# Kernel optimization log

Measured on AMD Instinct MI355X. Metric: run time of the kernel, lower is better.

The kernel has to match this reference:

```python
import jax, jax.numpy as jnp
import numpy as np
import math

SEQ = 45000
FEAT = 30
DEPTH, HEADS, DK, MLP, C = 4, 4, 32, 512, 32
MAXSEQ = 512


def pos_embed_table():
    # Enformer-style basis functions over distances [-SEQ+1, SEQ-1]
    d = jnp.arange(-SEQ + 1, SEQ, dtype=jnp.float32)
    a = jnp.abs(d)[:, None]
    nb = FEAT // 6  # basis per class (exponential / central-mask / gamma)
    # exponential decay
    hl = 2.0 ** jnp.linspace(3.0, math.log(SEQ) / math.log(2.0), nb)
    e1 = jnp.exp(-math.log(2.0) / hl[None, :] * a)
    # central mask
    cw = 2.0 ** jnp.arange(1, nb + 1, dtype=jnp.float32) - 1.0
    e2 = (cw[None, :] > a).astype(jnp.float32)
    # gamma pdf
    stddev = SEQ / (2 * nb)
    start_mean = SEQ / nb
    mean = jnp.linspace(start_mean, float(SEQ), nb)
    conc = (mean / stddev) ** 2
    rate = mean / stddev ** 2
    logp = jax.scipy.special.xlogy(conc - 1.0, a) - rate * a
    logz = jax.scipy.special.gammaln(conc) - conc * jnp.log(rate)
    p = jnp.exp(logp - logz) + 1e-8
    e3 = p / jnp.max(p)
    e = jnp.concatenate([e1, e2, e3], axis=-1)
    return jnp.concatenate([e, jnp.sign(d)[:, None] * e], axis=-1)  # [2*SEQ-1, FEAT]


def layernorm(x, g, b, eps=1e-5):
    mu = jnp.mean(x, axis=-1, keepdims=True)
    var = jnp.var(x, axis=-1, keepdims=True)
    return (x - mu) * jax.lax.rsqrt(var + eps) * g + b


def setup_inputs() -> dict:
    key = jax.random.key(0)
    ks = jax.random.split(key, 16)
    B, L = 2, SEQ
    HD = HEADS * DK
    s = 0.02
    return {
        "x_skip": jax.random.normal(ks[0], (B, C, L), jnp.float32),
        "attention": jax.random.uniform(ks[1], (B, 3, L), jnp.float32),
        "ln1_g": jnp.ones((DEPTH, C), jnp.float32),
        "ln1_b": jnp.zeros((DEPTH, C), jnp.float32),
        "Wq": jax.random.normal(ks[2], (DEPTH, C, HD), jnp.float32) * s,
        "Wk": jax.random.normal(ks[3], (DEPTH, C, HD), jnp.float32) * s,
        "Wv": jax.random.normal(ks[4], (DEPTH, C, HD), jnp.float32) * s,
        "Wrel": jax.random.normal(ks[5], (DEPTH, FEAT, HD), jnp.float32) * s,
        "rcb": jax.random.normal(ks[6], (DEPTH, HEADS, DK), jnp.float32),
        "rpb": jax.random.normal(ks[7], (DEPTH, HEADS, DK), jnp.float32),
        "Wo": jax.random.normal(ks[8], (DEPTH, HD, C), jnp.float32) * s,
        "bo": jnp.zeros((DEPTH, C), jnp.float32),
        "ln2_g": jnp.ones((DEPTH, C), jnp.float32),
        "ln2_b": jnp.zeros((DEPTH, C), jnp.float32),
        "W1": jax.random.normal(ks[9], (DEPTH, C, MLP), jnp.float32) * s,
        "b1": jnp.zeros((DEPTH, MLP), jnp.float32),
        "W2": jax.random.normal(ks[10], (DEPTH, MLP, C), jnp.float32) * s,
        "b2": jnp.zeros((DEPTH, C), jnp.float32),
    }


def reference(x_skip, attention, ln1_g, ln1_b, Wq, Wk, Wv, Wrel, rcb, rpb, Wo, bo, ln2_g, ln2_b, W1, b1, W2, b2):
    B, Cc, L = x_skip.shape
    half = MAXSEQ // 2
    x_emb = jnp.swapaxes(x_skip, 1, 2)  # [B, L, C]
    # top splice sites by acceptor / donor score
    acc = jnp.argsort(-attention[:, 1, :], axis=1)[:, :half]
    don = jnp.argsort(-attention[:, 2, :], axis=1)[:, :half]
    idx = jnp.sort(jnp.concatenate([acc, don], axis=1), axis=1)  # [B, n]
    n = idx.shape[1]
    diff = idx[:, :, None] - idx[:, None, :] + SEQ - 1  # [B, n, n]
    positions = pos_embed_table()[diff]  # [B, n, n, FEAT]
    emb = jnp.take_along_axis(x_emb, idx[:, :, None], axis=1)  # [B, n, C]
    scale = DK ** -0.5
    for l in range(DEPTH):
        h = layernorm(emb, ln1_g[l], ln1_b[l])
        q = (h @ Wq[l]).reshape(B, n, HEADS, DK).transpose(0, 2, 1, 3) * scale
        k = (h @ Wk[l]).reshape(B, n, HEADS, DK).transpose(0, 2, 1, 3)
        v = (h @ Wv[l]).reshape(B, n, HEADS, DK).transpose(0, 2, 1, 3)
        content = jnp.einsum('bhid,bhjd->bhij', q + rcb[l][None, :, None, :], k)
        rel_k = (positions @ Wrel[l]).reshape(B, n, n, HEADS, DK)  # b i j h d
        rel = jnp.einsum('bhid,bijhd->bhij', q + rpb[l][None, :, None, :], rel_k)
        attn_w = jax.nn.softmax(content + rel, axis=-1)
        o = jnp.einsum('bhij,bhjd->bhid', attn_w, v)
        o = o.transpose(0, 2, 1, 3).reshape(B, n, HEADS * DK)
        emb = emb + o @ Wo[l] + bo[l]
        h2 = layernorm(emb, ln2_g[l], ln2_b[l])
        emb = emb + jax.nn.gelu(h2 @ W1[l] + b1[l], approximate=False) @ W2[l] + b2[l]
    out = jnp.zeros_like(x_emb).at[jnp.arange(B)[:, None], idx].set(emb)
    return jnp.swapaxes(out, 1, 2)  # [B, C, L]
```

## Files before the change

### kernel.cpp

```cpp
#include <hip/hip_runtime.h>
#include <math.h>

#define SEQL   45000
#define NBAT   2
#define CCH    32
#define NSEL   512
#define NHEAD  4
#define DKD    32
#define HDD    128
#define MLPD   512
#define CDCAP  2048
#define TKB    32
#define ETB    176

__device__ __forceinline__ unsigned short f2bf(float x) {
  unsigned u = __float_as_uint(x);
  u = (u + 0x7fffu + ((u >> 16) & 1u)) >> 16;
  return (unsigned short)u;
}
#define BFL(u) __uint_as_float((u) << 16)
#define BFH(u) __uint_as_float((u) & 0xffff0000u)
#define U8F(w, s) ((float)(((w) >> (s)) & 0xffu))

__global__ __launch_bounds__(256) void prep_kernel(const float* __restrict__ att,
                                                   unsigned char* __restrict__ E,
                                                   int* __restrict__ hist,
                                                   float* __restrict__ out) {
  {
    int nthr = gridDim.x * 256;
    int gt = blockIdx.x * 256 + threadIdx.x;
    float4 z4 = make_float4(0.f, 0.f, 0.f, 0.f);
    float4* o4 = (float4*)out;
    for (int i = gt; i < NBAT * CCH * SEQL / 4; i += nthr) o4[i] = z4;
  }
  if (blockIdx.x < ETB) {
    int a = blockIdx.x * 256 + threadIdx.x;
    if (a >= SEQL) return;
    float ad = (float)a;
    float outv[16];
    float log2S = log2f((float)SEQL);
    #pragma unroll
    for (int k = 0; k < 5; ++k) {
      float hl = exp2f(3.0f + (float)k * (log2S - 3.0f) * 0.25f);
      outv[k] = exp2f(-ad / hl);
    }
    const int cw[5] = {1, 3, 7, 15, 31};
    #pragma unroll
    for (int k = 0; k < 5; ++k) outv[5 + k] = (a < cw[k]) ? 1.0f : 0.0f;
    float pmax = 0.0f;
    float pk[5];
    #pragma unroll
    for (int k = 0; k < 5; ++k) {
      float mean = 9000.0f * (float)(k + 1);
      float sd = 4500.0f;
      float cc = (mean / sd) * (mean / sd);
      float rr = mean / (sd * sd);
      float logz = lgammaf(cc) - cc * logf(rr);
      float pp;
      if (a == 0) pp = 1e-8f;
      else pp = expf((cc - 1.0f) * logf(ad) - rr * ad - logz) + 1e-8f;
      pk[k] = pp;
      float mstar = (cc - 1.0f) / rr;
      float m0 = floorf(mstar), m1 = m0 + 1.0f;
      if (m1 > (float)(SEQL - 1)) m1 = (float)(SEQL - 1);
      float p0 = expf((cc - 1.0f) * logf(m0) - rr * m0 - logz) + 1e-8f;
      float p1 = expf((cc - 1.0f) * logf(m1) - rr * m1 - logz) + 1e-8f;
      pmax = fmaxf(pmax, fmaxf(p0, p1));
    }
    #pragma unroll
    for (int k = 0; k < 5; ++k) outv[10 + k] = pk[k] / pmax;
    outv[15] = 0.0f;
    unsigned by[16];
    #pragma unroll
    for (int k = 0; k < 15; ++k)
      by[k] = (unsigned)(fminf(fmaxf(outv[k], 0.f), 1.f) * 255.f + 0.5f);
    by[15] = 0u;
    uint4 o;
    o.x = by[0]  | (by[1]  << 8) | (by[2]  << 16) | (by[3]  << 24);
    o.y = by[4]  | (by[5]  << 8) | (by[6]  << 16) | (by[7]  << 24);
    o.z = by[8]  | (by[9]  << 8) | (by[10] << 16) | (by[11] << 24);
    o.w = by[12] | (by[13] << 8) | (by[14] << 16);
    *(uint4*)(E + (size_t)a * 16) = o;
  } else {
    int bid = blockIdx.x - ETB;
    int ch4 = bid / TKB;
    int blk = bid % TKB;
    int b = ch4 >> 1, ch = ch4 & 1;
    const float* row = att + ((size_t)b * 3 + 1 + ch) * SEQL;
    int* h = hist + (size_t)ch4 * 65536;
    int per = (SEQL + TKB - 1) / TKB;
    int lo = blk * per;
    int hi = lo + per; if (hi > SEQL) hi = SEQL;
    for (int i = lo + threadIdx.x; i < hi; i += 256)
      atomicAdd(&h[__float_as_uint(row[i]) >> 16], 1);
  }
}

__global__ __launch_bounds__(256) void topk_collect_kernel(
    const float* __restrict__ att, const int* __restrict__ hist,
    unsigned long long* __restrict__ cand, int* __restrict__ cnt) {
  __shared__ int s_scan[256];
  __shared__ int s_aux[2];
  int tid = threadIdx.x;
  int ch4 = blockIdx.x / TKB;
  int blk = blockIdx.x % TKB;
  const int* h = hist + (size_t)ch4 * 65536;
  {
    int base = tid * 256;
    int sum = 0;
    for (int i = 0; i < 64; ++i) {
      int4 v = ((const int4*)(h + base))[i];
      sum += v.x + v.y + v.z + v.w;
    }
    s_scan[tid] = sum;
  }
  __syncthreads();
  for (int d = 1; d < 256; d <<= 1) {
    int v = s_scan[tid] + ((tid + d < 256) ? s_scan[tid + d] : 0);
    __syncthreads();
    s_scan[tid] = v;
    __syncthreads();
  }
  {
    int sufEx = (tid == 255) ? 0 : s_scan[tid + 1];
    if (s_scan[tid] >= 256 && sufEx < 256) { s_aux[0] = tid; s_aux[1] = 256 - sufEx; }
  }
  __syncthreads();
  int chunk = s_aux[0], want = s_aux[1];
  s_scan[tid] = h[chunk * 256 + tid];
  __syncthreads();
  for (int d = 1; d < 256; d <<= 1) {
    int v = s_scan[tid] + ((tid + d < 256) ? s_scan[tid + d] : 0);
    __syncthreads();
    s_scan[tid] = v;
    __syncthreads();
  }
  {
    int sufEx2 = (tid == 255) ? 0 : s_scan[tid + 1];
    if (s_scan[tid] >= want && sufEx2 < want) s_aux[0] = chunk * 256 + tid;
  }
  __syncthreads();
  unsigned T16 = (unsigned)s_aux[0];
  int b = ch4 >> 1, ch = ch4 & 1;
  const float* row = att + ((size_t)b * 3 + 1 + ch) * SEQL;
  int per = (SEQL + TKB - 1) / TKB;
  int lo = blk * per;
  int hi = lo + per; if (hi > SEQL) hi = SEQL;
  for (int i = lo + tid; i < hi; i += 256) {
    unsigned key = __float_as_uint(row[i]);
    if ((key >> 16) >= T16) {
      int p = atomicAdd(&cnt[ch4], 1);
      if (p < CDCAP)
        cand[(size_t)ch4 * CDCAP + p] =
            ((unsigned long long)key << 32) | (unsigned)(~(unsigned)i);
    }
  }
}

__global__ __launch_bounds__(1024) void topk_sort_kernel(
    const unsigned long long* __restrict__ cand, const int* __restrict__ cnt,
    unsigned* __restrict__ chsel) {
  __shared__ unsigned long long sc[CDCAP];
  int ch4 = blockIdx.x, t = threadIdx.x;
  int n = cnt[ch4]; if (n > CDCAP) n = CDCAP;
  int P = 256;
  while (P < n) P <<= 1;
  for (int i = t; i < P; i += 1024)
    sc[i] = (i < n) ? cand[(size_t)ch4 * CDCAP + i] : 0ull;
  __syncthreads();
  for (int k = 2; k <= P; k <<= 1) {
    for (int j = k >> 1; j > 0; j >>= 1) {
      for (int i = t; i < P; i += 1024) {
        int ixj = i ^ j;
        if (ixj > i) {
          unsigned long long va = sc[i], vb2 = sc[ixj];
          bool up = ((i & k) == 0);
          if ((va < vb2) == up) { sc[i] = vb2; sc[ixj] = va; }
        }
      }
      __syncthreads();
    }
  }
  if (t < 256)
    chsel[(size_t)ch4 * 256 + t] = ~(unsigned)(sc[t] & 0xFFFFFFFFull);
}

__global__ __launch_bounds__(512) void topk_merge_kernel(const unsigned* __restrict__ chsel,
                                                         int* __restrict__ idx) {
  __shared__ int m[512];
  int b = blockIdx.x, tid = threadIdx.x;
  m[tid] = (int)chsel[(size_t)b * 512 + tid];
  __syncthreads();
  for (int k = 2; k <= 512; k <<= 1) {
    for (int j = k >> 1; j > 0; j >>= 1) {
      int ixj = tid ^ j;
      if (ixj > tid) {
        int va = m[tid], vb2 = m[ixj];
        bool up = ((tid & k) == 0);
        if ((va > vb2) == up) { m[tid] = vb2; m[ixj] = va; }
      }
      __syncthreads();
    }
  }
  idx[b * 512 + tid] = m[tid];
}

__global__ __launch_bounds__(128) void gqkv0_kernel(
    const float* __restrict__ x, const int* __restrict__ idx,
    const float* __restrict__ ln_g, const float* __restrict__ ln_b,
    const float* __restrict__ Wq, const float* __restrict__ Wk,
    const float* __restrict__ Wv, const float* __restrict__ Wrel,
    const float* __restrict__ rcb, const float* __restrict__ rpb,
    float* __restrict__ emb, float* __restrict__ qc,
    unsigned short* __restrict__ kbT, unsigned short* __restrict__ vT,
    float* __restrict__ wb) {
  __shared__ float qs[128];
  const int l = 0;
  int hd = threadIdx.x;
  int hh = hd >> 5, d = hd & 31;
  int row = blockIdx.x;
  int b = row >> 9, ii = row & 511;
  int li = idx[b * NSEL + ii];
  float h[32];
  float mu = 0.f;
  #pragma unroll
  for (int c = 0; c < 32; ++c) {
    h[c] = x[((size_t)b * CCH + c) * SEQL + li];
    mu += h[c];
  }
  if (hd < 32) emb[(size_t)row * CCH + hd] = h[hd];
  mu *= (1.0f / 32.0f);
  float var = 0.f;
  #pragma unroll
  for (int c = 0; c < 32; ++c) { float dd0 = h[c] - mu; var += dd0 * dd0; }
  var *= (1.0f / 32.0f);
  float rstd = rsqrtf(var + 1e-5f);
  const float* g = ln_g + l * CCH;
  const float* bb = ln_b + l * CCH;
  #pragma unroll
  for (int c = 0; c < 32; ++c) h[c] = (h[c] - mu) * rstd * g[c] + bb[c];
  const float* wq = Wq + (size_t)l * CCH * HDD + hd;
  const float* wk = Wk + (size_t)l * CCH * HDD + hd;
  const float* wv = Wv + (size_t)l * CCH * HDD + hd;
  float q = 0.f, kk = 0.f, vv = 0.f;
  #pragma unroll
  for (int c = 0; c < 32; ++c) {
    q += h[c] * wq[c * HDD];
    kk += h[c] * wk[c * HDD];
    vv += h[c] * wv[c * HDD];
  }
  q *= 0.17677669529663687f;
  qs[hd] = q;
  qc[(size_t)row * HDD + hd] = q + rcb[(l * NHEAD + hh) * DKD + d];
  size_t tpos = ((size_t)(b * 4 + hh) * 4 + (d >> 3)) * 4096 + (size_t)ii * 8 + (d & 7);
  kbT[tpos] = f2bf(kk);
  vT[tpos]  = f2bf(vv);
  __syncthreads();
  if (hd < 120) {
    int h2 = hd / 30, f = hd % 30;
    const float* wr = Wrel + ((size_t)l * 30 + f) * HDD + h2 * DKD;
    const float* rp = rpb + (l * NHEAD + h2) * DKD;
    const float* qsh = qs + h2 * DKD;
    float acc = 0.f;
    #pragma unroll
    for (int dd = 0; dd < 32; ++dd) acc += (qsh[dd] + rp[dd]) * wr[dd];
    wb[((size_t)row * NHEAD + h2) * 32 + f] = acc;
  }
}

__global__ __launch_bounds__(256, 4) void attn_kernel(
    const float* __restrict__ qc, const unsigned short* __restrict__ kbT,
    const unsigned short* __restrict__ vT, const float* __restrict__ wbuf,
    const unsigned char* __restrict__ E, const int* __restrict__ idx,
    float* __restrict__ ob) {
  __shared__ float es[16 * 512];
  int bid = blockIdx.x;
  int b = bid >> 9;
  int i = bid & 511;
  int tid = threadIdx.x;
  int ii = idx[b * NSEL + i];
  #pragma unroll
  for (int rep = 0; rep < 2; ++rep) {
    int j = tid + rep * 256;
    int dj = ii - idx[b * NSEL + j];
    int a = dj < 0 ? -dj : dj;
    uint4 e = *(const uint4*)(E + (size_t)a * 16);
    es[0  * 512 + j] = U8F(e.x, 0);
    es[1  * 512 + j] = U8F(e.x, 8);
    es[2  * 512 + j] = U8F(e.x, 16);
    es[3  * 512 + j] = U8F(e.x, 24);
    es[4  * 512 + j] = U8F(e.y, 0);
    es[5  * 512 + j] = U8F(e.y, 8);
    es[6  * 512 + j] = U8F(e.y, 16);
    es[7  * 512 + j] = U8F(e.y, 24);
    es[8  * 512 + j] = U8F(e.z, 0);
    es[9  * 512 + j] = U8F(e.z, 8);
    es[10 * 512 + j] = U8F(e.z, 16);
    es[11 * 512 + j] = U8F(e.z, 24);
    es[12 * 512 + j] = U8F(e.w, 0);
    es[13 * 512 + j] = U8F(e.w, 8);
    es[14 * 512 + j] = U8F(e.w, 16);
    es[15 * 512 + j] = dj > 0 ? 1.f : (dj < 0 ? -1.f : 0.f);
  }
  __syncthreads();
  int h = tid >> 6, ln = tid & 63;
  const float* qrow = qc + (size_t)(b * NSEL + i) * HDD + h * DKD;
  float q[32];
  #pragma unroll
  for (int d4 = 0; d4 < 8; ++d4) {
    float4 qv = *(const float4*)(qrow + d4 * 4);
    q[d4 * 4 + 0] = qv.x; q[d4 * 4 + 1] = qv.y;
    q[d4 * 4 + 2] = qv.z; q[d4 * 4 + 3] = qv.w;
  }
  const float* wrow = wbuf + ((size_t)(b * NSEL + i) * NHEAD + h) * 32;
  float w0[15], w1[15];
  #pragma unroll
  for (int f = 0; f < 15; ++f) {
    w0[f] = wrow[f] * (1.0f / 255.0f);
    w1[f] = wrow[15 + f] * (1.0f / 255.0f);
  }
  const uint4* kb4 = (const uint4*)kbT + (size_t)(b * 4 + h) * 4 * 512;
  const uint4* vb4 = (const uint4*)vT + (size_t)(b * 4 + h) * 4 * 512;
  float lg[8];
  #pragma unroll
  for (int u = 0; u < 8; ++u) {
    int j = u * 64 + ln;
    float cacc = 0.f;
    #pragma unroll
    for (int dp = 0; dp < 4; ++dp) {
      uint4 kv = kb4[dp * 512 + j];
      cacc += q[dp * 8 + 0] * BFL(kv.x) + q[dp * 8 + 1] * BFH(kv.x)
            + q[dp * 8 + 2] * BFL(kv.y) + q[dp * 8 + 3] * BFH(kv.y)
            + q[dp * 8 + 4] * BFL(kv.z) + q[dp * 8 + 5] * BFH(kv.z)
            + q[dp * 8 + 6] * BFL(kv.w) + q[dp * 8 + 7] * BFH(kv.w);
    }
    float r0 = 0.f, r1 = 0.f;
    #pragma unroll
    for (int f = 0; f < 15; ++f) {
      float ef = es[f * 512 + j];
      r0 += ef * w0[f];
      r1 += ef * w1[f];
    }
    lg[u] = cacc + r0 + es[15 * 512 + j] * r1;
  }
  float m = lg[0];
  #pragma unroll
  for (int u = 1; u < 8; ++u) m = fmaxf(m, lg[u]);
  #pragma unroll
  for (int s = 1; s < 64; s <<= 1) m = fmaxf(m, __shfl_xor(m, s));
  float ssum = 0.f;
  #pragma unroll
  for (int u = 0; u < 8; ++u) { lg[u] = __expf(lg[u] - m); ssum += lg[u]; }
  #pragma unroll
  for (int s = 1; s < 64; s <<= 1) ssum += __shfl_xor(ssum, s);
  float invs = 1.0f / ssum;
  float* obrow = ob + (size_t)(b * NSEL + i) * HDD + h * DKD;
  #pragma unroll
  for (int dp = 0; dp < 4; ++dp) {
    float acc[8] = {0.f, 0.f, 0.f, 0.f, 0.f, 0.f, 0.f, 0.f};
    #pragma unroll
    for (int u = 0; u < 8; ++u) {
      uint4 vv = vb4[dp * 512 + u * 64 + ln];
      float p = lg[u];
      acc[0] += p * BFL(vv.x); acc[1] += p * BFH(vv.x);
      acc[2] += p * BFL(vv.y); acc[3] += p * BFH(vv.y);
      acc[4] += p * BFL(vv.z); acc[5] += p * BFH(vv.z);
      acc[6] += p * BFL(vv.w); acc[7] += p * BFH(vv.w);
    }
    #pragma unroll
    for (int s = 1; s < 8; s <<= 1) {
      #pragma unroll
      for (int t = 0; t < 8; ++t) acc[t] += __shfl_xor(acc[t], s);
    }
    int sel = ln & 7;
    float y = acc[0];
    #pragma unroll
    for (int t = 1; t < 8; ++t) y = (sel == t) ? acc[t] : y;
    #pragma unroll
    for (int s = 8; s < 64; s <<= 1) y += __shfl_xor(y, s);
    if (ln < 8) obrow[dp * 8 + ln] = y * invs;
  }
}

__global__ __launch_bounds__(256) void mlpqkv_kernel(
    const float* __restrict__ ob, const float* __restrict__ Wo,
    const float* __restrict__ bo,
    const float* __restrict__ ln2_g, const float* __restrict__ ln2_b,
    const float* __restrict__ W1, const float* __restrict__ b1,
    const float* __restrict__ W2, const float* __restrict__ b2,
    const float* __restrict__ ln1_g, const float* __restrict__ ln1_b,
    const float* __restrict__ Wq, const float* __restrict__ Wk,
    const float* __restrict__ Wv, const float* __restrict__ Wrel,
    const float* __restrict__ rcb, const float* __restrict__ rpb,
    const int* __restrict__ idx, float* __restrict__ emb,
    float* __restrict__ qc, unsigned short* __restrict__ kbT,
    unsigned short* __restrict__ vT, float* __restrict__ wb,
    float* __restrict__ out, int layer) {
  __shared__ float part[8][32];
  __shared__ float res[32];
  __shared__ float hln[32];
  __shared__ float fin[32];
  __shared__ float a1s[MLPD];
  __shared__ float qs[128];
  int row = blockIdx.x;
  int b = row >> 9, ii = row & 511;
  int tid = threadIdx.x;
  int c = tid & 31, seg = tid >> 5;
  const float* wo = Wo + (size_t)layer * HDD * CCH + c;
  const float* orow = ob + (size_t)row * HDD;
  float pacc = 0.f;
  #pragma unroll
  for (int k = 0; k < 16; ++k) {
    int kk = seg * 16 + k;
    pacc += orow[kk] * wo[kk * CCH];
  }
  part[seg][c] = pacc;
  __syncthreads();
  if (tid < 32) {
    float s = bo[layer * CCH + tid] + emb[(size_t)row * CCH + tid];
    #pragma unroll
    for (int sg = 0; sg < 8; ++sg) s += part[sg][tid];
    res[tid] = s;
  }
  __syncthreads();
  if (tid < 32) {
    float mu = 0.f, s2 = 0.f;
    #pragma unroll
    for (int c2 = 0; c2 < 32; ++c2) { float v = res[c2]; mu += v; s2 += v * v; }
    mu *= (1.0f / 32.0f);
    float var = s2 * (1.0f / 32.0f) - mu * mu;
    float rstd = rsqrtf(var + 1e-5f);
    hln[tid] = (res[tid] - mu) * rstd * ln2_g[layer * CCH + tid] + ln2_b[layer * CCH + tid];
  }
  __syncthreads();
  const float* w1 = W1 + (size_t)layer * CCH * MLPD;
  float accA = b1[layer * MLPD + tid];
  float accB = b1[layer * MLPD + tid + 256];
  for (int c2 = 0; c2 < 32; ++c2) {
    float hv = hln[c2];
    accA += hv * w1[c2 * MLPD + tid];
    accB += hv * w1[c2 * MLPD + tid + 256];
  }
  a1s[tid]       = 0.5f * accA * (1.0f + erff(accA * 0.70710678118654752f));
  a1s[tid + 256] = 0.5f * accB * (1.0f + erff(accB * 0.70710678118654752f));
  __syncthreads();
  const float* w2 = W2 + (size_t)layer * MLPD * CCH;
  float acc2 = 0.f;
  #pragma unroll 4
  for (int mi = 0; mi < 64; ++mi) {
    int m = seg * 64 + mi;
    acc2 += a1s[m] * w2[m * CCH + c];
  }
  __syncthreads();
  part[seg][c] = acc2;
  __syncthreads();
  if (tid < 32) {
    float s = b2[layer * CCH + tid] + res[tid];
    #pragma unroll
    for (int sg = 0; sg < 8; ++sg) s += part[sg][tid];
    fin[tid] = s;
    if (layer < 3) emb[(size_t)row * CCH + tid] = s;
  }
  __syncthreads();
  if (layer == 3) {
    if (tid < 32) {
      int li = idx[b * NSEL + ii];
      out[((size_t)b * CCH + tid) * SEQL + li] = fin[tid];
    }
    return;
  }
  const int l1 = layer + 1;
  bool act = tid < 128;
  int hd = tid & 127;
  int hh = hd >> 5, d = hd & 31;
  if (act) {
    float h[32];
    float mu = 0.f;
    #pragma unroll
    for (int c2 = 0; c2 < 32; ++c2) { h[c2] = fin[c2]; mu += h[c2]; }
    mu *= (1.0f / 32.0f);
    float var = 0.f;
    #pragma unroll
    for (int c2 = 0; c2 < 32; ++c2) { float dd = h[c2] - mu; var += dd * dd; }
    var *= (1.0f / 32.0f);
    float rstd = rsqrtf(var + 1e-5f);
    const float* g = ln1_g + l1 * CCH;
    const float* bb = ln1_b + l1 * CCH;
    #pragma unroll
    for (int c2 = 0; c2 < 32; ++c2) h[c2] = (h[c2] - mu) * rstd * g[c2] + bb[c2];
    const float* wq = Wq + (size_t)l1 * CCH * HDD + hd;
    const float* wk = Wk + (size_t)l1 * CCH * HDD + hd;
    const float* wv = Wv + (size_t)l1 * CCH * HDD + hd;
    float q = 0.f, kk = 0.f, vv = 0.f;
    #pragma unroll
    for (int c2 = 0; c2 < 32; ++c2) {
      q += h[c2] * wq[c2 * HDD];
      kk += h[c2] * wk[c2 * HDD];
      vv += h[c2] * wv[c2 * HDD];
    }
    q *= 0.17677669529663687f;
    qs[hd] = q;
    qc[(size_t)row * HDD + hd] = q + rcb[(l1 * NHEAD + hh) * DKD + d];
    size_t tpos = ((size_t)(b * 4 + hh) * 4 + (d >> 3)) * 4096 + (size_t)ii * 8 + (d & 7);
    kbT[tpos] = f2bf(kk);
    vT[tpos]  = f2bf(vv);
  }
  __syncthreads();
  if (act && hd < 120) {
    int h2 = hd / 30, f = hd % 30;
    const float* rp = rpb + (l1 * NHEAD + h2) * DKD;
    const float* wr = Wrel + ((size_t)l1 * 30 + f) * HDD + h2 * DKD;
    const float* qsh = qs + h2 * DKD;
    float acc = 0.f;
    #pragma unroll
    for (int dd = 0; dd < 32; ++dd) acc += (qsh[dd] + rp[dd]) * wr[dd];
    wb[((size_t)row * NHEAD + h2) * 32 + f] = acc;
  }
}

extern "C" void kernel_launch(void* const* d_in, const int* in_sizes, int n_in,
                              void* d_out, int out_size, void* d_ws, size_t ws_size,
                              hipStream_t stream) {
  (void)in_sizes; (void)n_in; (void)ws_size; (void)out_size;
  const float* x_skip    = (const float*)d_in[0];
  const float* attention = (const float*)d_in[1];
  const float* ln1_g = (const float*)d_in[2];
  const float* ln1_b = (const float*)d_in[3];
  const float* Wq    = (const float*)d_in[4];
  const float* Wk    = (const float*)d_in[5];
  const float* Wv    = (const float*)d_in[6];
  const float* Wrel  = (const float*)d_in[7];
  const float* rcb   = (const float*)d_in[8];
  const float* rpb   = (const float*)d_in[9];
  const float* Wo    = (const float*)d_in[10];
  const float* bo    = (const float*)d_in[11];
  const float* ln2_g = (const float*)d_in[12];
  const float* ln2_b = (const float*)d_in[13];
  const float* W1    = (const float*)d_in[14];
  const float* b1    = (const float*)d_in[15];
  const float* W2    = (const float*)d_in[16];
  const float* b2    = (const float*)d_in[17];
  float* out = (float*)d_out;
  char* ws = (char*)d_ws;

  unsigned char* E = (unsigned char*)(ws + 0);
  int*      idx   = (int*)(ws + 1441792);
  float*    emb   = (float*)(ws + 1445888);
  float*    qc    = (float*)(ws + 1576960);
  unsigned short* kbT = (unsigned short*)(ws + 2101248);
  unsigned short* vT  = (unsigned short*)(ws + 2363392);
  float*    wb    = (float*)(ws + 2625536);
  float*    ob    = (float*)(ws + 3149824);
  int*      hist  = (int*)(ws + 3674112);
  int*      cnt   = (int*)(ws + 4722688);
  unsigned long long* cand = (unsigned long long*)(ws + 4722720);
  unsigned* chsel = (unsigned*)(ws + 4788256);

  hipMemsetAsync(ws + 3674112, 0, 1048576 + 32, stream);
  prep_kernel<<<ETB + 4 * TKB, 256, 0, stream>>>(attention, E, hist, out);
  topk_collect_kernel<<<4 * TKB, 256, 0, stream>>>(attention, hist, cand, cnt);
  topk_sort_kernel<<<4, 1024, 0, stream>>>(cand, cnt, chsel);
  topk_merge_kernel<<<2, 512, 0, stream>>>(chsel, idx);
  gqkv0_kernel<<<1024, 128, 0, stream>>>(x_skip, idx, ln1_g, ln1_b, Wq, Wk, Wv,
                                         Wrel, rcb, rpb, emb, qc, kbT, vT, wb);
  for (int l = 0; l < 4; ++l) {
    attn_kernel<<<1024, 256, 0, stream>>>(qc, kbT, vT, wb, E, idx, ob);
    mlpqkv_kernel<<<1024, 256, 0, stream>>>(ob, Wo, bo, ln2_g, ln2_b, W1, b1,
                                            W2, b2, ln1_g, ln1_b, Wq, Wk, Wv,
                                            Wrel, rcb, rpb, idx, emb, qc, kbT,
                                            vT, wb, out, l);
  }
}
```

Baseline: 325.0 us.

## Fuse attention and MLP/QKV kernels per layer with ping-pong buffers

```diff
diff --git a/kernel.cpp b/kernel.cpp
--- a/kernel.cpp
+++ b/kernel.cpp
@@ -268,21 +268,38 @@
   }
 }
 
-__global__ __launch_bounds__(256, 4) void attn_kernel(
+__global__ __launch_bounds__(256, 4) void layer_kernel(
     const float* __restrict__ qc, const unsigned short* __restrict__ kbT,
     const unsigned short* __restrict__ vT, const float* __restrict__ wbuf,
     const unsigned char* __restrict__ E, const int* __restrict__ idx,
-    float* __restrict__ ob) {
+    const float* __restrict__ Wo, const float* __restrict__ bo,
+    const float* __restrict__ ln2_g, const float* __restrict__ ln2_b,
+    const float* __restrict__ W1, const float* __restrict__ b1,
+    const float* __restrict__ W2, const float* __restrict__ b2,
+    const float* __restrict__ ln1_g, const float* __restrict__ ln1_b,
+    const float* __restrict__ Wq, const float* __restrict__ Wk,
+    const float* __restrict__ Wv, const float* __restrict__ Wrel,
+    const float* __restrict__ rcb, const float* __restrict__ rpb,
+    float* __restrict__ emb, float* __restrict__ qcN,
+    unsigned short* __restrict__ kbTN, unsigned short* __restrict__ vTN,
+    float* __restrict__ wbN, float* __restrict__ out, int layer) {
   __shared__ float es[16 * 512];
+  __shared__ float obs[128];
+  __shared__ float part[8][32];
+  __shared__ float res[32];
+  __shared__ float hln[32];
+  __shared__ float fin[32];
+  __shared__ float a1s[MLPD];
+  __shared__ float qs[128];
   int bid = blockIdx.x;
   int b = bid >> 9;
   int i = bid & 511;
   int tid = threadIdx.x;
-  int ii = idx[b * NSEL + i];
+  int pos = idx[b * NSEL + i];
   #pragma unroll
   for (int rep = 0; rep < 2; ++rep) {
     int j = tid + rep * 256;
-    int dj = ii - idx[b * NSEL + j];
+    int dj = pos - idx[b * NSEL + j];
     int a = dj < 0 ? -dj : dj;
     uint4 e = *(const uint4*)(E + (size_t)a * 16);
     es[0  * 512 + j] = U8F(e.x, 0);
@@ -303,121 +320,99 @@
     es[15 * 512 + j] = dj > 0 ? 1.f : (dj < 0 ? -1.f : 0.f);
   }
   __syncthreads();
-  int h = tid >> 6, ln = tid & 63;
-  const float* qrow = qc + (size_t)(b * NSEL + i) * HDD + h * DKD;
-  float q[32];
-  #pragma unroll
-  for (int d4 = 0; d4 < 8; ++d4) {
-    float4 qv = *(const float4*)(qrow + d4 * 4);
-    q[d4 * 4 + 0] = qv.x; q[d4 * 4 + 1] = qv.y;
-    q[d4 * 4 + 2] = qv.z; q[d4 * 4 + 3] = qv.w;
-  }
-  const float* wrow = wbuf + ((size_t)(b * NSEL + i) * NHEAD + h) * 32;
-  float w0[15], w1[15];
-  #pragma unroll
-  for (int f = 0; f < 15; ++f) {
-    w0[f] = wrow[f] * (1.0f / 255.0f);
-    w1[f] = wrow[15 + f] * (1.0f / 255.0f);
-  }
-  const uint4* kb4 = (const uint4*)kbT + (size_t)(b * 4 + h) * 4 * 512;
-  const uint4* vb4 = (const uint4*)vT + (size_t)(b * 4 + h) * 4 * 512;
-  float lg[8];
-  #pragma unroll
-  for (int u = 0; u < 8; ++u) {
-    int j = u * 64 + ln;
-    float cacc = 0.f;
+  {
+    int h = tid >> 6, ln = tid & 63;
+    const float* qrow = qc + (size_t)(b * NSEL + i) * HDD + h * DKD;
+    float q[32];
+    #pragma unroll
+    for (int d4 = 0; d4 < 8; ++d4) {
+      float4 qv = *(const float4*)(qrow + d4 * 4);
+      q[d4 * 4 + 0] = qv.x; q[d4 * 4 + 1] = qv.y;
+      q[d4 * 4 + 2] = qv.z; q[d4 * 4 + 3] = qv.w;
+    }
+    const float* wrow = wbuf + ((size_t)(b * NSEL + i) * NHEAD + h) * 32;
+    float w0[15], w1[15];
+    #pragma unroll
+    for (int f = 0; f < 15; ++f) {
+      w0[f] = wrow[f] * (1.0f / 255.0f);
+      w1[f] = wrow[15 + f] * (1.0f / 255.0f);
+    }
+    const uint4* kb4 = (const uint4*)kbT + (size_t)(b * 4 + h) * 4 * 512;
+    const uint4* vb4 = (const uint4*)vT + (size_t)(b * 4 + h) * 4 * 512;
+    float lg[8];
+    #pragma unroll
+    for (int u = 0; u < 8; ++u) {
+      int j = u * 64 + ln;
+      float cacc = 0.f;
+      #pragma unroll
+      for (int dp = 0; dp < 4; ++dp) {
+        uint4 kv = kb4[dp * 512 + j];
+        cacc += q[dp * 8 + 0] * BFL(kv.x) + q[dp * 8 + 1] * BFH(kv.x)
+              + q[dp * 8 + 2] * BFL(kv.y) + q[dp * 8 + 3] * BFH(kv.y)
+              + q[dp * 8 + 4] * BFL(kv.z) + q[dp * 8 + 5] * BFH(kv.z)
+              + q[dp * 8 + 6] * BFL(kv.w) + q[dp * 8 + 7] * BFH(kv.w);
+      }
+      float r0 = 0.f, r1 = 0.f;
+      #pragma unroll
+      for (int f = 0; f < 15; ++f) {
+        float ef = es[f * 512 + j];
+        r0 += ef * w0[f];
+        r1 += ef * w1[f];
+      }
+      lg[u] = cacc + r0 + es[15 * 512 + j] * r1;
+    }
+    float m = lg[0];
+    #pragma unroll
+    for (int u = 1; u < 8; ++u) m = fmaxf(m, lg[u]);
+    #pragma unroll
+    for (int s = 1; s < 64; s <<= 1) m = fmaxf(m, __shfl_xor(m, s));
+    float ssum = 0.f;
+    #pragma unroll
+    for (int u = 0; u < 8; ++u) { lg[u] = __expf(lg[u] - m); ssum += lg[u]; }
+    #pragma unroll
+    for (int s = 1; s < 64; s <<= 1) ssum += __shfl_xor(ssum, s);
+    float invs = 1.0f / ssum;
     #pragma unroll
     for (int dp = 0; dp < 4; ++dp) {
-      uint4 kv = kb4[dp * 512 + j];
-      cacc += q[dp * 8 + 0] * BFL(kv.x) + q[dp * 8 + 1] * BFH(kv.x)
-            + q[dp * 8 + 2] * BFL(kv.y) + q[dp * 8 + 3] * BFH(kv.y)
-            + q[dp * 8 + 4] * BFL(kv.z) + q[dp * 8 + 5] * BFH(kv.z)
-            + q[dp * 8 + 6] * BFL(kv.w) + q[dp * 8 + 7] * BFH(kv.w);
-    }
-    float r0 = 0.f, r1 = 0.f;
-    #pragma unroll
-    for (int f = 0; f < 15; ++f) {
-      float ef = es[f * 512 + j];
-      r0 += ef * w0[f];
-      r1 += ef * w1[f];
-    }
-    lg[u] = cacc + r0 + es[15 * 512 + j] * r1;
-  }
-  float m = lg[0];
-  #pragma unroll
-  for (int u = 1; u < 8; ++u) m = fmaxf(m, lg[u]);
-  #pragma unroll
-  for (int s = 1; s < 64; s <<= 1) m = fmaxf(m, __shfl_xor(m, s));
-  float ssum = 0.f;
-  #pragma unroll
-  for (int u = 0; u < 8; ++u) { lg[u] = __expf(lg[u] - m); ssum += lg[u]; }
-  #pragma unroll
-  for (int s = 1; s < 64; s <<= 1) ssum += __shfl_xor(ssum, s);
-  float invs = 1.0f / ssum;
-  float* obrow = ob + (size_t)(b * NSEL + i) * HDD + h * DKD;
-  #pragma unroll
-  for (int dp = 0; dp < 4; ++dp) {
-    float acc[8] = {0.f, 0.f, 0.f, 0.f, 0.f, 0.f, 0.f, 0.f};
-    #pragma unroll
-    for (int u = 0; u < 8; ++u) {
-      uint4 vv = vb4[dp * 512 + u * 64 + ln];
-      float p = lg[u];
-      acc[0] += p * BFL(vv.x); acc[1] += p * BFH(vv.x);
-      acc[2] += p * BFL(vv.y); acc[3] += p * BFH(vv.y);
-      acc[4] += p * BFL(vv.z); acc[5] += p * BFH(vv.z);
-      acc[6] += p * BFL(vv.w); acc[7] += p * BFH(vv.w);
-    }
-    #pragma unroll
-    for (int s = 1; s < 8; s <<= 1) {
+      float acc[8] = {0.f, 0.f, 0.f, 0.f, 0.f, 0.f, 0.f, 0.f};
       #pragma unroll
-      for (int t = 0; t < 8; ++t) acc[t] += __shfl_xor(acc[t], s);
-    }
-    int sel = ln & 7;
-    float y = acc[0];
-    #pragma unroll
-    for (int t = 1; t < 8; ++t) y = (sel == t) ? acc[t] : y;
-    #pragma unroll
-    for (int s = 8; s < 64; s <<= 1) y += __shfl_xor(y, s);
-    if (ln < 8) obrow[dp * 8 + ln] = y * invs;
-  }
-}
-
-__global__ __launch_bounds__(256) void mlpqkv_kernel(
-    const float* __restrict__ ob, const float* __restrict__ Wo,
-    const float* __restrict__ bo,
-    const float* __restrict__ ln2_g, const float* __restrict__ ln2_b,
-    const float* __restrict__ W1, const float* __restrict__ b1,
-    const float* __restrict__ W2, const float* __restrict__ b2,
-    const float* __restrict__ ln1_g, const float* __restrict__ ln1_b,
-    const float* __restrict__ Wq, const float* __restrict__ Wk,
-    const float* __restrict__ Wv, const float* __restrict__ Wrel,
-    const float* __restrict__ rcb, const float* __restrict__ rpb,
-    const int* __restrict__ idx, float* __restrict__ emb,
-    float* __restrict__ qc, unsigned short* __restrict__ kbT,
-    unsigned short* __restrict__ vT, float* __restrict__ wb,
-    float* __restrict__ out, int layer) {
-  __shared__ float part[8][32];
-  __shared__ float res[32];
-  __shared__ float hln[32];
-  __shared__ float fin[32];
-  __shared__ float a1s[MLPD];
-  __shared__ float qs[128];
-  int row = blockIdx.x;
-  int b = row >> 9, ii = row & 511;
-  int tid = threadIdx.x;
+      for (int u = 0; u < 8; ++u) {
+        uint4 vv = vb4[dp * 512 + u * 64 + ln];
+        float p = lg[u];
+        acc[0] += p * BFL(vv.x); acc[1] += p * BFH(vv.x);
+        acc[2] += p * BFL(vv.y); acc[3] += p * BFH(vv.y);
+        acc[4] += p * BFL(vv.z); acc[5] += p * BFH(vv.z);
+        acc[6] += p * BFL(vv.w); acc[7] += p * BFH(vv.w);
+      }
+      #pragma unroll
+      for (int s = 1; s < 8; s <<= 1) {
+        #pragma unroll
+        for (int t = 0; t < 8; ++t) acc[t] += __shfl_xor(acc[t], s);
+      }
+      int sel = ln & 7;
+      float y = acc[0];
+      #pragma unroll
+      for (int t = 1; t < 8; ++t) y = (sel == t) ? acc[t] : y;
+      #pragma unroll
+      for (int s = 8; s < 64; s <<= 1) y += __shfl_xor(y, s);
+      if (ln < 8) obs[h * DKD + dp * 8 + ln] = y * invs;
+    }
+  }
+  __syncthreads();
   int c = tid & 31, seg = tid >> 5;
-  const float* wo = Wo + (size_t)layer * HDD * CCH + c;
-  const float* orow = ob + (size_t)row * HDD;
-  float pacc = 0.f;
-  #pragma unroll
-  for (int k = 0; k < 16; ++k) {
-    int kk = seg * 16 + k;
-    pacc += orow[kk] * wo[kk * CCH];
-  }
-  part[seg][c] = pacc;
+  {
+    const float* wo = Wo + (size_t)layer * HDD * CCH + c;
+    float pacc = 0.f;
+    #pragma unroll
+    for (int k = 0; k < 16; ++k) {
+      int kk = seg * 16 + k;
+      pacc += obs[kk] * wo[kk * CCH];
+    }
+    part[seg][c] = pacc;
+  }
   __syncthreads();
   if (tid < 32) {
-    float s = bo[layer * CCH + tid] + emb[(size_t)row * CCH + tid];
+    float s = bo[layer * CCH + tid] + emb[(size_t)bid * CCH + tid];
     #pragma unroll
     for (int sg = 0; sg < 8; ++sg) s += part[sg][tid];
     res[tid] = s;
@@ -433,77 +428,78 @@
     hln[tid] = (res[tid] - mu) * rstd * ln2_g[layer * CCH + tid] + ln2_b[layer * CCH + tid];
   }
   __syncthreads();
-  const float* w1 = W1 + (size_t)layer * CCH * MLPD;
-  float accA = b1[layer * MLPD + tid];
-  float accB = b1[layer * MLPD + tid + 256];
-  for (int c2 = 0; c2 < 32; ++c2) {
-    float hv = hln[c2];
-    accA += hv * w1[c2 * MLPD + tid];
-    accB += hv * w1[c2 * MLPD + tid + 256];
-  }
-  a1s[tid]       = 0.5f * accA * (1.0f + erff(accA * 0.70710678118654752f));
-  a1s[tid + 256] = 0.5f * accB * (1.0f + erff(accB * 0.70710678118654752f));
-  __syncthreads();
-  const float* w2 = W2 + (size_t)layer * MLPD * CCH;
-  float acc2 = 0.f;
-  #pragma unroll 4
-  for (int mi = 0; mi < 64; ++mi) {
-    int m = seg * 64 + mi;
-    acc2 += a1s[m] * w2[m * CCH + c];
-  }
-  __syncthreads();
-  part[seg][c] = acc2;
+  {
+    const float* w1 = W1 + (size_t)layer * CCH * MLPD;
+    float accA = b1[layer * MLPD + tid];
+    float accB = b1[layer * MLPD + tid + 256];
+    for (int c2 = 0; c2 < 32; ++c2) {
+      float hv = hln[c2];
+      accA += hv * w1[c2 * MLPD + tid];
+      accB += hv * w1[c2 * MLPD + tid + 256];
+    }
+    a1s[tid]       = 0.5f * accA * (1.0f + erff(accA * 0.70710678118654752f));
+    a1s[tid + 256] = 0.5f * accB * (1.0f + erff(accB * 0.70710678118654752f));
+  }
+  __syncthreads();
+  {
+    const float* w2 = W2 + (size_t)layer * MLPD * CCH;
+    float acc2 = 0.f;
+    #pragma unroll 4
+    for (int mi = 0; mi < 64; ++mi) {
+      int m = seg * 64 + mi;
+      acc2 += a1s[m] * w2[m * CCH + c];
+    }
+    __syncthreads();
+    part[seg][c] = acc2;
+  }
   __syncthreads();
   if (tid < 32) {
     float s = b2[layer * CCH + tid] + res[tid];
     #pragma unroll
     for (int sg = 0; sg < 8; ++sg) s += part[sg][tid];
     fin[tid] = s;
-    if (layer < 3) emb[(size_t)row * CCH + tid] = s;
+    if (layer < 3) emb[(size_t)bid * CCH + tid] = s;
   }
   __syncthreads();
   if (layer == 3) {
-    if (tid < 32) {
-      int li = idx[b * NSEL + ii];
-      out[((size_t)b * CCH + tid) * SEQL + li] = fin[tid];
-    }
+    if (tid < 32) out[((size_t)b * CCH + tid) * SEQL + pos] = fin[tid];
     return;
   }
   const int l1 = layer + 1;
   bool act = tid < 128;
   int hd = tid & 127;
-  int hh = hd >> 5, d = hd & 31;
+  int hh2 = hd >> 5, dd2 = hd & 31;
   if (act) {
-    float h[32];
+    float hx[32];
     float mu = 0.f;
     #pragma unroll
-    for (int c2 = 0; c2 < 32; ++c2) { h[c2] = fin[c2]; mu += h[c2]; }
+    for (int c2 = 0; c2 < 32; ++c2) { hx[c2] = fin[c2]; mu += hx[c2]; }
     mu *= (1.0f / 32.0f);
     float var = 0.f;
     #pragma unroll
-    for (int c2 = 0; c2 < 32; ++c2) { float dd = h[c2] - mu; var += dd * dd; }
+    for (int c2 = 0; c2 < 32; ++c2) { float dd = hx[c2] - mu; var += dd * dd; }
     var *= (1.0f / 32.0f);
     float rstd = rsqrtf(var + 1e-5f);
     const float* g = ln1_g + l1 * CCH;
     const float* bb = ln1_b + l1 * CCH;
     #pragma unroll
-    for (int c2 = 0; c2 < 32; ++c2) h[c2] = (h[c2] - mu) * rstd * g[c2] + bb[c2];
+    for (int c2 = 0; c2 < 32; ++c2) hx[c2] = (hx[c2] - mu) * rstd * g[c2] + bb[c2];
     const float* wq = Wq + (size_t)l1 * CCH * HDD + hd;
     const float* wk = Wk + (size_t)l1 * CCH * HDD + hd;
     const float* wv = Wv + (size_t)l1 * CCH * HDD + hd;
     float q = 0.f, kk = 0.f, vv = 0.f;
     #pragma unroll
     for (int c2 = 0; c2 < 32; ++c2) {
-      q += h[c2] * wq[c2 * HDD];
-      kk += h[c2] * wk[c2 * HDD];
-      vv += h[c2] * wv[c2 * HDD];
+      q += hx[c2] * wq[c2 * HDD];
+      kk += hx[c2] * wk[c2 * HDD];
+      vv += hx[c2] * wv[c2 * HDD];
     }
     q *= 0.17677669529663687f;
     qs[hd] = q;
-    qc[(size_t)row * HDD + hd] = q + rcb[(l1 * NHEAD + hh) * DKD + d];
-    size_t tpos = ((size_t)(b * 4 + hh) * 4 + (d >> 3)) * 4096 + (size_t)ii * 8 + (d & 7);
-    kbT[tpos] = f2bf(kk);
-    vT[tpos]  = f2bf(vv);
+    qcN[(size_t)bid * HDD + hd] = q + rcb[(l1 * NHEAD + hh2) * DKD + dd2];
+    size_t tpos = ((size_t)(b * 4 + hh2) * 4 + (dd2 >> 3)) * 4096 + (size_t)i * 8 + (dd2 & 7);
+    kbTN[tpos] = f2bf(kk);
+    vTN[tpos]  = f2bf(vv);
   }
   __syncthreads();
   if (act && hd < 120) {
@@ -514,7 +510,7 @@
     float acc = 0.f;
     #pragma unroll
     for (int dd = 0; dd < 32; ++dd) acc += (qsh[dd] + rp[dd]) * wr[dd];
-    wb[((size_t)row * NHEAD + h2) * 32 + f] = acc;
+    wbN[((size_t)bid * NHEAD + h2) * 32 + f] = acc;
   }
 }
 
@@ -546,15 +542,18 @@
   unsigned char* E = (unsigned char*)(ws + 0);
   int*      idx   = (int*)(ws + 1441792);
   float*    emb   = (float*)(ws + 1445888);
-  float*    qc    = (float*)(ws + 1576960);
-  unsigned short* kbT = (unsigned short*)(ws + 2101248);
-  unsigned short* vT  = (unsigned short*)(ws + 2363392);
-  float*    wb    = (float*)(ws + 2625536);
-  float*    ob    = (float*)(ws + 3149824);
+  float*    qcA   = (float*)(ws + 1576960);
+  unsigned short* kbTA = (unsigned short*)(ws + 2101248);
+  unsigned short* vTA  = (unsigned short*)(ws + 2363392);
+  float*    wbA   = (float*)(ws + 2625536);
+  unsigned short* kbTB = (unsigned short*)(ws + 3149824);
+  unsigned short* vTB  = (unsigned short*)(ws + 3411968);
   int*      hist  = (int*)(ws + 3674112);
   int*      cnt   = (int*)(ws + 4722688);
   unsigned long long* cand = (unsigned long long*)(ws + 4722720);
   unsigned* chsel = (unsigned*)(ws + 4788256);
+  float*    qcB   = (float*)(ws + 4792352);
+  float*    wbB   = (float*)(ws + 5316640);
 
   hipMemsetAsync(ws + 3674112, 0, 1048576 + 32, stream);
   prep_kernel<<<ETB + 4 * TKB, 256, 0, stream>>>(attention, E, hist, out);
@@ -562,12 +561,19 @@
   topk_sort_kernel<<<4, 1024, 0, stream>>>(cand, cnt, chsel);
   topk_merge_kernel<<<2, 512, 0, stream>>>(chsel, idx);
   gqkv0_kernel<<<1024, 128, 0, stream>>>(x_skip, idx, ln1_g, ln1_b, Wq, Wk, Wv,
-                                         Wrel, rcb, rpb, emb, qc, kbT, vT, wb);
+                                         Wrel, rcb, rpb, emb, qcA, kbTA, vTA, wbA);
   for (int l = 0; l < 4; ++l) {
-    attn_kernel<<<1024, 256, 0, stream>>>(qc, kbT, vT, wb, E, idx, ob);
-    mlpqkv_kernel<<<1024, 256, 0, stream>>>(ob, Wo, bo, ln2_g, ln2_b, W1, b1,
-                                            W2, b2, ln1_g, ln1_b, Wq, Wk, Wv,
-                                            Wrel, rcb, rpb, idx, emb, qc, kbT,
-                                            vT, wb, out, l);
-  }
-}
+    const float* qcI = (l & 1) ? qcB : qcA;
+    const unsigned short* kbI = (l & 1) ? kbTB : kbTA;
+    const unsigned short* vI  = (l & 1) ? vTB : vTA;
+    const float* wbI = (l & 1) ? wbB : wbA;
+    float* qcO = (l & 1) ? qcA : qcB;
+    unsigned short* kbO = (l & 1) ? kbTA : kbTB;
+    unsigned short* vO  = (l & 1) ? vTA : vTB;
+    float* wbO = (l & 1) ? wbA : wbB;
+    layer_kernel<<<1024, 256, 0, stream>>>(qcI, kbI, vI, wbI, E, idx,
+                                           Wo, bo, ln2_g, ln2_b, W1, b1, W2, b2,
+                                           ln1_g, ln1_b, Wq, Wk, Wv, Wrel, rcb,
+                                           rpb, emb, qcO, kbO, vO, wbO, out, l);
+  }
+}
```

After: 306.9 us. 5.6% less time.
